# Kernel tuning notes

Measured on AMD Instinct MI355X. Metric: run time of the kernel, lower is better.

Reference implementation:

```python
import jax, jax.numpy as jnp
import numpy as np

B, P, F, C = 32, 1024, 512, 512  # graphs, max nodes (pad target), feat dim, args.num_node
EVRATIO = 0.1

def setup_inputs() -> dict:
    key = jax.random.key(0)
    k1, k2, k3 = jax.random.split(key, 3)
    num_vertices = jax.random.randint(k1, (B,), 512, P + 1, dtype=jnp.int32)  # ragged sizes N_i
    node_mask = jnp.arange(P)[None, :] < num_vertices[:, None]  # [B,P]
    x = jax.random.normal(k2, (B, P, F), dtype=jnp.float32) * node_mask[:, :, None]
    # per-graph eigenvector matrix, zero-padded to [P,P] (rows=nodes, cols=spectral idx)
    evec = jax.random.normal(k3, (B, P, P), dtype=jnp.float32) * (P ** -0.5)
    evectors = evec * node_mask[:, :, None] * node_mask[:, None, :]
    return {"x": x, "evectors": evectors, "num_vertices": num_vertices}


def reference(x, evectors, num_vertices):
    # dropout is identity in eval mode
    Nf = num_vertices.astype(jnp.float32)

    # --- transformed_evectors: select C evenly spaced spectral columns, pad rows to P, transpose
    step = (Nf - 1.0) / (C - 1)                                   # [B]
    idx = jnp.round(jnp.arange(C, dtype=jnp.float32)[None, :] * step[:, None]).astype(jnp.int32)
    sel = jnp.take_along_axis(evectors, idx[:, None, :].repeat(P, axis=1), axis=2)  # [B,P,C]
    updated_evectors = jnp.transpose(sel, (0, 2, 1))              # [B,C,P]

    # --- GFT: gft = evec.T @ x per graph (zero padding keeps invalid rows/cols at 0)
    gft = jnp.einsum('bnp,bnf->bpf', evectors, x)                 # [B,P,F]

    # --- data-dependent 3-way split along spectral axis, expressed as masks
    s1 = jnp.ceil(Nf * EVRATIO).astype(jnp.int32)
    s2 = jnp.ceil(Nf * EVRATIO * 2.0).astype(jnp.int32)
    bounds = jnp.stack([jnp.zeros_like(s1), s1, s1 + s2, num_vertices], axis=1)  # [B,4]
    p_ids = jnp.arange(P)
    masks = ((p_ids[None, None, :] >= bounds[:, :3, None]) &
             (p_ids[None, None, :] < bounds[:, 1:, None])).astype(x.dtype)       # [B,3,P]

    # updated part k = evec[:, slice_k] @ gft[slice_k]; concat along node axis -> stacked [B,3,P,F]
    x_updated = jnp.einsum('bnp,bkp,bpf->bknf', evectors, masks, gft)            # [B,3,P,F]

    original_x = jnp.broadcast_to(x[:, None], x_updated.shape)

    n_level_feat = x
    return (n_level_feat, x_updated, original_x, updated_evectors)
```

## Files before the change

### kernel.cpp

```cpp
#include <hip/hip_runtime.h>
#include <hip/hip_bf16.h>

#define B_ 32
#define P_ 1024
#define F_ 512
#define C_ 512

#define BM 128
#define BN 128
#define BK 64

typedef unsigned short u16;
typedef unsigned int   u32;
typedef __bf16 bf16x8 __attribute__((ext_vector_type(8)));
typedef float  f32x4  __attribute__((ext_vector_type(4)));

union U4 { uint4 v; u16 h[8]; u32 w[4]; };

__device__ __forceinline__ u16 f2bf(float f) {
  u32 x = __builtin_bit_cast(u32, f);
  return (u16)((x + 0x7FFFu + ((x >> 16) & 1u)) >> 16);
}
__device__ __forceinline__ u32 pack2(float a, float b) {
  return (u32)f2bf(a) | ((u32)f2bf(b) << 16);
}

__device__ __forceinline__ f32x4 mfma16(bf16x8 a, bf16x8 b, f32x4 c) {
  return __builtin_amdgcn_mfma_f32_16x16x32_bf16(a, b, c, 0, 0, 0);
}

__device__ __forceinline__ int swzc(int m, int c) { return m * 8 + (c ^ (m & 7)); }

__device__ __forceinline__ void gload16(const u16* g, u16* l) {
  __builtin_amdgcn_global_load_lds((const __attribute__((address_space(1))) void*)(g),
                                   (__attribute__((address_space(3))) void*)(l), 16, 0, 0);
}

__global__ __launch_bounds__(256) void copy_kernel(const uint4* __restrict__ x,
                                                   uint4* __restrict__ out0,
                                                   uint4* __restrict__ out2) {
  int i = blockIdx.x * 256 + threadIdx.x;
  uint4 v = x[i];
  out0[i] = v;
  int b = i >> 17;
  int r = i & 131071;
  uint4* o2 = out2 + ((size_t)b * 3 * 131072 + r);
  o2[0] = v; o2[131072] = v; o2[2 * 131072] = v;
}

__global__ __launch_bounds__(256) void sel_kernel(const float* __restrict__ evec,
                                                  const int* __restrict__ nv,
                                                  float* __restrict__ out3) {
  const int b  = blockIdx.z;
  const int c0 = blockIdx.y * 64;
  const int p0 = blockIdx.x * 64;
  const int N  = nv[b];
  const float step = (float)(N - 1) / 511.0f;
  const int base  = (int)rintf((float)c0 * step);
  const int basea = base & ~3;
  __shared__ float tile[64][145];
  const int t = threadIdx.x;

  for (int it = t; it < 64 * 36; it += 256) {
    int row = it / 36, g = it % 36;
    int colg = basea + g * 4;
    const float* src = evec + ((size_t)b * P_ + (p0 + row)) * P_ + colg;
    if (colg + 4 <= P_) {
      float4 v = *(const float4*)src;
      tile[row][g * 4 + 0] = v.x;
      tile[row][g * 4 + 1] = v.y;
      tile[row][g * 4 + 2] = v.z;
      tile[row][g * 4 + 3] = v.w;
    } else {
      #pragma unroll
      for (int j = 0; j < 4; ++j)
        tile[row][g * 4 + j] = (colg + j < P_) ? src[j] : 0.f;
    }
  }
  __syncthreads();

  for (int it = t; it < 64 * 32; it += 256) {
    int cl = it >> 5, pp = it & 31;
    int c = c0 + cl;
    int col = (int)rintf((float)c * step) - basea;
    float2 val = make_float2(tile[pp * 2][col], tile[pp * 2 + 1][col]);
    *(float2*)(out3 + ((size_t)b * C_ + c) * P_ + p0 + pp * 2) = val;
  }
}

__global__ __launch_bounds__(256) void castE(const float* __restrict__ evec,
                                             u16* __restrict__ evecb,
                                             u16* __restrict__ evecT) {
  const int b = blockIdx.z, n0 = blockIdx.y * 64, p0 = blockIdx.x * 64;
  __shared__ float tile[64][66];
  const int t = threadIdx.x;
  #pragma unroll
  for (int q = 0; q < 4; ++q) {
    int id = q * 256 + t;
    int row = id >> 4, c4 = (id & 15) * 4;
    float4 v = *(const float4*)(evec + ((size_t)b * P_ + n0 + row) * P_ + p0 + c4);
    u32 pr[2] = { pack2(v.x, v.y), pack2(v.z, v.w) };
    *(uint2*)(evecb + ((size_t)b * P_ + n0 + row) * P_ + p0 + c4) = *(uint2*)pr;
    *(float2*)&tile[row][c4]     = make_float2(v.x, v.y);
    *(float2*)&tile[row][c4 + 2] = make_float2(v.z, v.w);
  }
  __syncthreads();
  #pragma unroll
  for (int q = 0; q < 4; ++q) {
    int id = q * 256 + t;
    int pr = id >> 4, c4 = (id & 15) * 4;
    u32 o[2];
    o[0] = pack2(tile[c4 + 0][pr], tile[c4 + 1][pr]);
    o[1] = pack2(tile[c4 + 2][pr], tile[c4 + 3][pr]);
    *(uint2*)(evecT + ((size_t)b * P_ + p0 + pr) * P_ + n0 + c4) = *(uint2*)o;
  }
}

__global__ __launch_bounds__(256) void castX(const float* __restrict__ x,
                                             u16* __restrict__ xT) {
  const int b = blockIdx.z, n0 = blockIdx.x * 64, f0 = blockIdx.y * 64;
  __shared__ float tile[64][66];
  const int t = threadIdx.x;
  #pragma unroll
  for (int q = 0; q < 4; ++q) {
    int id = q * 256 + t;
    int row = id >> 4, c4 = (id & 15) * 4;
    float4 v = *(const float4*)(x + ((size_t)b * P_ + n0 + row) * F_ + f0 + c4);
    *(float2*)&tile[row][c4]     = make_float2(v.x, v.y);
    *(float2*)&tile[row][c4 + 2] = make_float2(v.z, v.w);
  }
  __syncthreads();
  #pragma unroll
  for (int q = 0; q < 4; ++q) {
    int id = q * 256 + t;
    int fr = id >> 4, c4 = (id & 15) * 4;
    u32 o[2];
    o[0] = pack2(tile[c4 + 0][fr], tile[c4 + 1][fr]);
    o[1] = pack2(tile[c4 + 2][fr], tile[c4 + 3][fr]);
    *(uint2*)(xT + ((size_t)b * F_ + f0 + fr) * P_ + n0 + c4) = *(uint2*)o;
  }
}

__device__ __forceinline__ void mma_tile(const u16* lA, const u16* lB,
                                         int wm, int wn, int lrow, int quad,
                                         f32x4 acc[4][4]) {
  #pragma unroll
  for (int ks = 0; ks < 2; ++ks) {
    bf16x8 af[4], bfr[4];
    #pragma unroll
    for (int mi = 0; mi < 4; ++mi)
      af[mi] = *(const bf16x8*)(lA + swzc(wm + mi * 16 + lrow, ks * 4 + quad) * 8);
    #pragma unroll
    for (int ni = 0; ni < 4; ++ni)
      bfr[ni] = *(const bf16x8*)(lB + swzc(wn + ni * 16 + lrow, ks * 4 + quad) * 8);
    #pragma unroll
    for (int mi = 0; mi < 4; ++mi)
      #pragma unroll
      for (int ni = 0; ni < 4; ++ni)
        acc[mi][ni] = mfma16(af[mi], bfr[ni], acc[mi][ni]);
  }
}

__global__ __launch_bounds__(256) void gemm1(const u16* __restrict__ xT,
                                             const u16* __restrict__ evecT,
                                             const int* __restrict__ nv,
                                             u16* __restrict__ gftT) {
  const int b = blockIdx.z, m0 = blockIdx.x * BM, p0 = blockIdx.y * BN;
  const int N = nv[b];
  __shared__ __align__(16) u16 lA[BM * 64];
  __shared__ __align__(16) u16 lB[BN * 64];
  f32x4 acc[4][4] = {};
  const int t = threadIdx.x, lane = t & 63, w = t >> 6;
  const int wm = (w >> 1) * 64, wn = (w & 1) * 64;
  const int lrow = lane & 15, quad = lane >> 4;

  for (int kk = 0; kk < N; kk += BK) {
    #pragma unroll
    for (int q = 0; q < 4; ++q) {
      int s = q * 256 + t, m = s >> 3, csrc = (s & 7) ^ (m & 7);
      u16* ldst = lA + (q * 256 + (t & 192)) * 8;
      gload16(xT + ((size_t)b * F_ + m0 + m) * P_ + kk + csrc * 8, ldst);
      gload16(evecT + ((size_t)b * P_ + p0 + m) * P_ + kk + csrc * 8,
              lB + (q * 256 + (t & 192)) * 8);
    }
    __syncthreads();
    mma_tile(lA, lB, wm, wn, lrow, quad, acc);
    __syncthreads();
  }

  #pragma unroll
  for (int mi = 0; mi < 4; ++mi)
    #pragma unroll
    for (int ni = 0; ni < 4; ++ni) {
      int row = m0 + wm + mi * 16 + quad * 4;
      int col = p0 + wn + ni * 16 + lrow;
      u16* dst = gftT + ((size_t)b * F_ + row) * P_ + col;
      #pragma unroll
      for (int r = 0; r < 4; ++r) dst[(size_t)r * P_] = f2bf(acc[mi][ni][r]);
    }
}

__global__ __launch_bounds__(256) void gemm2(const u16* __restrict__ evecb,
                                             const u16* __restrict__ gftT,
                                             const int* __restrict__ nv,
                                             float* __restrict__ out1) {
  const int b = blockIdx.z / 3, slab = blockIdx.z % 3;
  const int m0 = blockIdx.x * BM, f0 = blockIdx.y * BN;
  const int N = nv[b];
  const float t1 = (float)N * 0.1f;
  const int s1 = (int)ceilf(t1);
  const int s2 = (int)ceilf(t1 * 2.0f);
  const int lo = (slab == 0) ? 0 : ((slab == 1) ? s1 : s1 + s2);
  const int hi = (slab == 0) ? s1 : ((slab == 1) ? s1 + s2 : N);

  __shared__ __align__(16) u16 lA[BM * 64];
  __shared__ __align__(16) u16 lB[BN * 64];
  f32x4 acc[4][4] = {};
  const int t = threadIdx.x, lane = t & 63, w = t >> 6;
  const int wm = (w >> 1) * 64, wn = (w & 1) * 64;
  const int lrow = lane & 15, quad = lane >> 4;

  for (int kk = (lo & ~(BK - 1)); kk < hi; kk += BK) {
    #pragma unroll
    for (int q = 0; q < 4; ++q) {
      int s = q * 256 + t, m = s >> 3, csrc = (s & 7) ^ (m & 7);
      gload16(evecb + ((size_t)b * P_ + m0 + m) * P_ + kk + csrc * 8,
              lA + (q * 256 + (t & 192)) * 8);
    }
    if (kk >= lo && kk + BK <= hi) {
      #pragma unroll
      for (int q = 0; q < 4; ++q) {
        int s = q * 256 + t, m = s >> 3, csrc = (s & 7) ^ (m & 7);
        gload16(gftT + ((size_t)b * F_ + f0 + m) * P_ + kk + csrc * 8,
                lB + (q * 256 + (t & 192)) * 8);
      }
    } else {
      #pragma unroll
      for (int q = 0; q < 4; ++q) {
        int s = q * 256 + t, m = s >> 3, c = s & 7;
        int kb = kk + c * 8;
        U4 u;
        u.v = *(const uint4*)(gftT + ((size_t)b * F_ + f0 + m) * P_ + kb);
        if (kb < lo || kb + 8 > hi) {
          #pragma unroll
          for (int j = 0; j < 8; ++j)
            if (kb + j < lo || kb + j >= hi) u.h[j] = 0;
        }
        *(uint4*)(lB + swzc(m, c) * 8) = u.v;
      }
    }
    __syncthreads();
    mma_tile(lA, lB, wm, wn, lrow, quad, acc);
    __syncthreads();
  }

  #pragma unroll
  for (int mi = 0; mi < 4; ++mi)
    #pragma unroll
    for (int ni = 0; ni < 4; ++ni) {
      int row = m0 + wm + mi * 16 + quad * 4;
      int col = f0 + wn + ni * 16 + lrow;
      float* dst = out1 + (((size_t)b * 3 + slab) * P_ + row) * F_ + col;
      #pragma unroll
      for (int r = 0; r < 4; ++r) dst[(size_t)r * F_] = acc[mi][ni][r];
    }
}

extern "C" void kernel_launch(void* const* d_in, const int* in_sizes, int n_in,
                              void* d_out, int out_size, void* d_ws, size_t ws_size,
                              hipStream_t stream) {
  const float* x  = nullptr;
  const float* ev = nullptr;
  const int*   nv = nullptr;
  for (int i = 0; i < n_in; ++i) {
    if      (in_sizes[i] == B_)            nv = (const int*)d_in[i];
    else if (in_sizes[i] == B_ * P_ * P_)  ev = (const float*)d_in[i];
    else if (in_sizes[i] == B_ * P_ * F_)  x  = (const float*)d_in[i];
  }

  float* out = (float*)d_out;
  const size_t S0 = (size_t)B_ * P_ * F_;
  float* out0 = out;
  float* out1 = out + S0;
  float* out2 = out + 4 * S0;
  float* out3 = out + 7 * S0;

  u16* gftT  = (u16*)d_ws;
  u16* evecT = gftT  + (size_t)B_ * F_ * P_;
  u16* evecb = evecT + (size_t)B_ * P_ * P_;
  u16* xT    = evecb + (size_t)B_ * P_ * P_;

  copy_kernel<<<16384, 256, 0, stream>>>((const uint4*)x, (uint4*)out0, (uint4*)out2);
  sel_kernel<<<dim3(16, 8, 32), 256, 0, stream>>>(ev, nv, out3);
  castX<<<dim3(16, 8, 32), 256, 0, stream>>>(x, xT);
  castE<<<dim3(16, 16, 32), 256, 0, stream>>>(ev, evecb, evecT);
  gemm1<<<dim3(4, 8, 32), 256, 0, stream>>>(xT, evecT, nv, gftT);
  gemm2<<<dim3(8, 4, 96), 256, 0, stream>>>(evecb, gftT, nv, out1);
}
```

Baseline: 822.9 us.

## Double-buffer GEMM LDS tiles, fuse x copies into cast, read selection from bf16

Both GEMMs now double-buffer their LDS tiles, prefetching the next K tile while MFMAs run on the current one. In gemm2 the masked boundary tiles are staged through registers and written to LDS after the math. The standalone copy kernel is folded into the x transpose/cast kernel so x is read once. The evector column selection now gathers rows of the bf16 transposed copy instead of the fp32 input. That cuts read traffic but returns bf16-rounded values for that output, which risks accuracy.

```diff
diff --git a/kernel.cpp b/kernel.cpp
--- a/kernel.cpp
+++ b/kernel.cpp
@@ -24,6 +24,10 @@
 __device__ __forceinline__ u32 pack2(float a, float b) {
   return (u32)f2bf(a) | ((u32)f2bf(b) << 16);
 }
+__device__ __forceinline__ float bf2f(u16 h) {
+  u32 x = (u32)h << 16;
+  return __builtin_bit_cast(float, x);
+}
 
 __device__ __forceinline__ f32x4 mfma16(bf16x8 a, bf16x8 b, f32x4 c) {
   return __builtin_amdgcn_mfma_f32_16x16x32_bf16(a, b, c, 0, 0, 0);
@@ -34,58 +38,6 @@
 __device__ __forceinline__ void gload16(const u16* g, u16* l) {
   __builtin_amdgcn_global_load_lds((const __attribute__((address_space(1))) void*)(g),
                                    (__attribute__((address_space(3))) void*)(l), 16, 0, 0);
-}
-
-__global__ __launch_bounds__(256) void copy_kernel(const uint4* __restrict__ x,
-                                                   uint4* __restrict__ out0,
-                                                   uint4* __restrict__ out2) {
-  int i = blockIdx.x * 256 + threadIdx.x;
-  uint4 v = x[i];
-  out0[i] = v;
-  int b = i >> 17;
-  int r = i & 131071;
-  uint4* o2 = out2 + ((size_t)b * 3 * 131072 + r);
-  o2[0] = v; o2[131072] = v; o2[2 * 131072] = v;
-}
-
-__global__ __launch_bounds__(256) void sel_kernel(const float* __restrict__ evec,
-                                                  const int* __restrict__ nv,
-                                                  float* __restrict__ out3) {
-  const int b  = blockIdx.z;
-  const int c0 = blockIdx.y * 64;
-  const int p0 = blockIdx.x * 64;
-  const int N  = nv[b];
-  const float step = (float)(N - 1) / 511.0f;
-  const int base  = (int)rintf((float)c0 * step);
-  const int basea = base & ~3;
-  __shared__ float tile[64][145];
-  const int t = threadIdx.x;
-
-  for (int it = t; it < 64 * 36; it += 256) {
-    int row = it / 36, g = it % 36;
-    int colg = basea + g * 4;
-    const float* src = evec + ((size_t)b * P_ + (p0 + row)) * P_ + colg;
-    if (colg + 4 <= P_) {
-      float4 v = *(const float4*)src;
-      tile[row][g * 4 + 0] = v.x;
-      tile[row][g * 4 + 1] = v.y;
-      tile[row][g * 4 + 2] = v.z;
-      tile[row][g * 4 + 3] = v.w;
-    } else {
-      #pragma unroll
-      for (int j = 0; j < 4; ++j)
-        tile[row][g * 4 + j] = (colg + j < P_) ? src[j] : 0.f;
-    }
-  }
-  __syncthreads();
-
-  for (int it = t; it < 64 * 32; it += 256) {
-    int cl = it >> 5, pp = it & 31;
-    int c = c0 + cl;
-    int col = (int)rintf((float)c * step) - basea;
-    float2 val = make_float2(tile[pp * 2][col], tile[pp * 2 + 1][col]);
-    *(float2*)(out3 + ((size_t)b * C_ + c) * P_ + p0 + pp * 2) = val;
-  }
 }
 
 __global__ __launch_bounds__(256) void castE(const float* __restrict__ evec,
@@ -116,8 +68,10 @@
   }
 }
 
-__global__ __launch_bounds__(256) void castX(const float* __restrict__ x,
-                                             u16* __restrict__ xT) {
+__global__ __launch_bounds__(256) void castX_copy(const float* __restrict__ x,
+                                                  u16* __restrict__ xT,
+                                                  float* __restrict__ out0,
+                                                  float* __restrict__ out2) {
   const int b = blockIdx.z, n0 = blockIdx.x * 64, f0 = blockIdx.y * 64;
   __shared__ float tile[64][66];
   const int t = threadIdx.x;
@@ -125,7 +79,13 @@
   for (int q = 0; q < 4; ++q) {
     int id = q * 256 + t;
     int row = id >> 4, c4 = (id & 15) * 4;
-    float4 v = *(const float4*)(x + ((size_t)b * P_ + n0 + row) * F_ + f0 + c4);
+    size_t src = ((size_t)b * P_ + n0 + row) * F_ + f0 + c4;
+    float4 v = *(const float4*)(x + src);
+    *(float4*)(out0 + src) = v;
+    size_t d2 = (((size_t)b * 3) * P_ + n0 + row) * F_ + f0 + c4;
+    *(float4*)(out2 + d2) = v;
+    *(float4*)(out2 + d2 + (size_t)P_ * F_) = v;
+    *(float4*)(out2 + d2 + 2 * (size_t)P_ * F_) = v;
     *(float2*)&tile[row][c4]     = make_float2(v.x, v.y);
     *(float2*)&tile[row][c4 + 2] = make_float2(v.z, v.w);
   }
@@ -141,6 +101,24 @@
   }
 }
 
+__global__ __launch_bounds__(256) void sel_kernel(const u16* __restrict__ evecT,
+                                                  const int* __restrict__ nv,
+                                                  float* __restrict__ out3) {
+  const int b = blockIdx.y, c0 = blockIdx.x * 4, t = threadIdx.x;
+  const int N = nv[b];
+  const float step = (float)(N - 1) / 511.0f;
+  #pragma unroll
+  for (int r = 0; r < 4; ++r) {
+    int c = c0 + r;
+    int idx = (int)rintf((float)c * step);
+    uint2 v = *(const uint2*)(evecT + ((size_t)b * P_ + idx) * P_ + t * 4);
+    float4 o;
+    o.x = bf2f((u16)(v.x & 0xffffu)); o.y = bf2f((u16)(v.x >> 16));
+    o.z = bf2f((u16)(v.y & 0xffffu)); o.w = bf2f((u16)(v.y >> 16));
+    *(float4*)(out3 + ((size_t)b * C_ + c) * P_ + t * 4) = o;
+  }
+}
+
 __device__ __forceinline__ void mma_tile(const u16* lA, const u16* lB,
                                          int wm, int wn, int lrow, int quad,
                                          f32x4 acc[4][4]) {
@@ -158,6 +136,23 @@
       #pragma unroll
       for (int ni = 0; ni < 4; ++ni)
         acc[mi][ni] = mfma16(af[mi], bfr[ni], acc[mi][ni]);
+  }
+}
+
+__device__ __forceinline__ void stage2(const u16* gA, const u16* gB,
+                                       u16* lA, u16* lB, int t) {
+  #pragma unroll
+  for (int q = 0; q < 4; ++q) {
+    int s = q * 256 + t, m = s >> 3, csrc = (s & 7) ^ (m & 7);
+    gload16(gA + (size_t)m * P_ + csrc * 8, lA + (q * 256 + (t & 192)) * 8);
+    gload16(gB + (size_t)m * P_ + csrc * 8, lB + (q * 256 + (t & 192)) * 8);
+  }
+}
+__device__ __forceinline__ void stage1op(const u16* g, u16* l, int t) {
+  #pragma unroll
+  for (int q = 0; q < 4; ++q) {
+    int s = q * 256 + t, m = s >> 3, csrc = (s & 7) ^ (m & 7);
+    gload16(g + (size_t)m * P_ + csrc * 8, l + (q * 256 + (t & 192)) * 8);
   }
 }
 
@@ -167,25 +162,25 @@
                                              u16* __restrict__ gftT) {
   const int b = blockIdx.z, m0 = blockIdx.x * BM, p0 = blockIdx.y * BN;
   const int N = nv[b];
-  __shared__ __align__(16) u16 lA[BM * 64];
-  __shared__ __align__(16) u16 lB[BN * 64];
+  __shared__ __align__(16) u16 lA[2][BM * BK];
+  __shared__ __align__(16) u16 lB[2][BN * BK];
   f32x4 acc[4][4] = {};
   const int t = threadIdx.x, lane = t & 63, w = t >> 6;
   const int wm = (w >> 1) * 64, wn = (w & 1) * 64;
   const int lrow = lane & 15, quad = lane >> 4;
-
-  for (int kk = 0; kk < N; kk += BK) {
-    #pragma unroll
-    for (int q = 0; q < 4; ++q) {
-      int s = q * 256 + t, m = s >> 3, csrc = (s & 7) ^ (m & 7);
-      u16* ldst = lA + (q * 256 + (t & 192)) * 8;
-      gload16(xT + ((size_t)b * F_ + m0 + m) * P_ + kk + csrc * 8, ldst);
-      gload16(evecT + ((size_t)b * P_ + p0 + m) * P_ + kk + csrc * 8,
-              lB + (q * 256 + (t & 192)) * 8);
-    }
+  const u16* gA = xT + ((size_t)b * F_ + m0) * P_;
+  const u16* gB = evecT + ((size_t)b * P_ + p0) * P_;
+  const int nt = (N + BK - 1) / BK;
+
+  stage2(gA, gB, lA[0], lB[0], t);
+  __syncthreads();
+  int cur = 0;
+  for (int ti = 0; ti < nt; ++ti) {
+    if (ti + 1 < nt)
+      stage2(gA + (ti + 1) * BK, gB + (ti + 1) * BK, lA[cur ^ 1], lB[cur ^ 1], t);
+    mma_tile(lA[cur], lB[cur], wm, wn, lrow, quad, acc);
     __syncthreads();
-    mma_tile(lA, lB, wm, wn, lrow, quad, acc);
-    __syncthreads();
+    cur ^= 1;
   }
 
   #pragma unroll
@@ -213,45 +208,69 @@
   const int lo = (slab == 0) ? 0 : ((slab == 1) ? s1 : s1 + s2);
   const int hi = (slab == 0) ? s1 : ((slab == 1) ? s1 + s2 : N);
 
-  __shared__ __align__(16) u16 lA[BM * 64];
-  __shared__ __align__(16) u16 lB[BN * 64];
+  __shared__ __align__(16) u16 lA[2][BM * BK];
+  __shared__ __align__(16) u16 lB[2][BN * BK];
   f32x4 acc[4][4] = {};
   const int t = threadIdx.x, lane = t & 63, w = t >> 6;
   const int wm = (w >> 1) * 64, wn = (w & 1) * 64;
   const int lrow = lane & 15, quad = lane >> 4;
-
-  for (int kk = (lo & ~(BK - 1)); kk < hi; kk += BK) {
-    #pragma unroll
-    for (int q = 0; q < 4; ++q) {
-      int s = q * 256 + t, m = s >> 3, csrc = (s & 7) ^ (m & 7);
-      gload16(evecb + ((size_t)b * P_ + m0 + m) * P_ + kk + csrc * 8,
-              lA + (q * 256 + (t & 192)) * 8);
-    }
-    if (kk >= lo && kk + BK <= hi) {
-      #pragma unroll
-      for (int q = 0; q < 4; ++q) {
-        int s = q * 256 + t, m = s >> 3, csrc = (s & 7) ^ (m & 7);
-        gload16(gftT + ((size_t)b * F_ + f0 + m) * P_ + kk + csrc * 8,
-                lB + (q * 256 + (t & 192)) * 8);
-      }
+  const u16* gA = evecb + ((size_t)b * P_ + m0) * P_;
+  const u16* gB = gftT + ((size_t)b * F_ + f0) * P_;
+  const int kstart = lo & ~(BK - 1);
+  const int nt = (hi - kstart + BK - 1) / BK;
+
+  {
+    stage1op(gA + kstart, lA[0], t);
+    if (kstart >= lo && kstart + BK <= hi) {
+      stage1op(gB + kstart, lB[0], t);
     } else {
       #pragma unroll
       for (int q = 0; q < 4; ++q) {
         int s = q * 256 + t, m = s >> 3, c = s & 7;
-        int kb = kk + c * 8;
-        U4 u;
-        u.v = *(const uint4*)(gftT + ((size_t)b * F_ + f0 + m) * P_ + kb);
-        if (kb < lo || kb + 8 > hi) {
+        int kb = kstart + c * 8;
+        U4 u; u.v = *(const uint4*)(gB + (size_t)m * P_ + kb);
+        #pragma unroll
+        for (int j = 0; j < 8; ++j)
+          if (kb + j < lo || kb + j >= hi) u.h[j] = 0;
+        *(uint4*)(lB[0] + swzc(m, c) * 8) = u.v;
+      }
+    }
+  }
+  __syncthreads();
+
+  int cur = 0;
+  for (int ti = 0; ti < nt; ++ti) {
+    const int kn = kstart + (ti + 1) * BK;
+    const bool have = (ti + 1 < nt);
+    bool nb = false;
+    U4 breg[4];
+    if (have) {
+      stage1op(gA + kn, lA[cur ^ 1], t);
+      nb = !(kn >= lo && kn + BK <= hi);
+      if (!nb) {
+        stage1op(gB + kn, lB[cur ^ 1], t);
+      } else {
+        #pragma unroll
+        for (int q = 0; q < 4; ++q) {
+          int s = q * 256 + t, m = s >> 3, c = s & 7;
+          int kb = kn + c * 8;
+          breg[q].v = *(const uint4*)(gB + (size_t)m * P_ + kb);
           #pragma unroll
           for (int j = 0; j < 8; ++j)
-            if (kb + j < lo || kb + j >= hi) u.h[j] = 0;
+            if (kb + j < lo || kb + j >= hi) breg[q].h[j] = 0;
         }
-        *(uint4*)(lB + swzc(m, c) * 8) = u.v;
       }
     }
+    mma_tile(lA[cur], lB[cur], wm, wn, lrow, quad, acc);
+    if (have && nb) {
+      #pragma unroll
+      for (int q = 0; q < 4; ++q) {
+        int s = q * 256 + t, m = s >> 3, c = s & 7;
+        *(uint4*)(lB[cur ^ 1] + swzc(m, c) * 8) = breg[q].v;
+      }
+    }
     __syncthreads();
-    mma_tile(lA, lB, wm, wn, lrow, quad, acc);
-    __syncthreads();
+    cur ^= 1;
   }
 
   #pragma unroll
@@ -290,10 +309,9 @@
   u16* evecb = evecT + (size_t)B_ * P_ * P_;
   u16* xT    = evecb + (size_t)B_ * P_ * P_;
 
-  copy_kernel<<<16384, 256, 0, stream>>>((const uint4*)x, (uint4*)out0, (uint4*)out2);
-  sel_kernel<<<dim3(16, 8, 32), 256, 0, stream>>>(ev, nv, out3);
-  castX<<<dim3(16, 8, 32), 256, 0, stream>>>(x, xT);
   castE<<<dim3(16, 16, 32), 256, 0, stream>>>(ev, evecb, evecT);
+  castX_copy<<<dim3(16, 8, 32), 256, 0, stream>>>(x, xT, out0, out2);
+  sel_kernel<<<dim3(128, 32), 256, 0, stream>>>(evecT, nv, out3);
   gemm1<<<dim3(4, 8, 32), 256, 0, stream>>>(xT, evecT, nv, gftT);
   gemm2<<<dim3(8, 4, 96), 256, 0, stream>>>(evecb, gftT, nv, out1);
 }
```

After: 795.4 us. 1.03x faster.
